# Kernel optimization log

Measured on AMD Instinct MI355X. Metric: run time of the kernel, lower is better.

Reference implementation:

```python
import jax, jax.numpy as jnp
import numpy as np

E, H = 300, 256          # embedding_dim, GRU hidden per direction
D = 2 * H                # BiGRU output / GCN feature dim
V, PAD = 30000, 0
B, T_LEN, C_LEN = 128, 50, 200
N_GCN = 2
OUT = 3


def _gru_dir(x, Wih, Whh, bih, bhh):
    # x: [B,S,E] -> [B,S,H]; torch GRU equations
    h0 = jnp.zeros((x.shape[0], Whh.shape[1]), x.dtype)
    def step(h, xt):
        gi = xt @ Wih.T + bih                 # [B,3H]
        gh = h @ Whh.T + bhh
        ir, iz, inn = jnp.split(gi, 3, axis=-1)
        hr, hz, hn = jnp.split(gh, 3, axis=-1)
        r = jax.nn.sigmoid(ir + hr)
        z = jax.nn.sigmoid(iz + hz)
        n = jnp.tanh(inn + r * hn)
        hnew = (1.0 - z) * n + z * h
        return hnew, hnew
    _, hs = jax.lax.scan(step, h0, jnp.swapaxes(x, 0, 1))
    return jnp.swapaxes(hs, 0, 1)


def _bigru(x, wih, whh, bih, bhh):
    # wih:[2,3H,E] whh:[2,3H,H] bih/bhh:[2,3H]
    f = _gru_dir(x, wih[0], whh[0], bih[0], bhh[0])
    b = _gru_dir(x[:, ::-1], wih[1], whh[1], bih[1], bhh[1])[:, ::-1]
    return jnp.concatenate([f, b], axis=-1)   # [B,S,2H]


def _stance_attn(tgt_emb, clm_emb, gt, gc):
    tgt_ht = _bigru(tgt_emb, *gt)
    clm_ht = _bigru(clm_emb, *gc)
    tgt_last = tgt_ht[:, -1]
    # 'dot' attention: weight[b,c] = claim_ht[b,c] . target_last_ht[b]
    w = jnp.einsum('bcd,bd->bc', clm_ht, tgt_last)
    # NOTE: original `weight.masked_fill(mask==0, -1e9)` result is DISCARDED
    # (non-inplace torch op), so the mask has no effect -> faithfully omitted.
    return tgt_ht, clm_ht, jax.nn.softmax(w, axis=1)


def _gcn(tgt_ht, clm_ht, Ws):
    # StanceGCN: cat nodes, N_GCN layers of dot-correlation attention + residual relu
    node = jnp.concatenate([tgt_ht, clm_ht], axis=1)   # [B,N,D]
    T = tgt_ht.shape[1]
    for i in range(Ws.shape[0]):
        # dot correlation reduces to pairwise inner products (no [B,N,N,D] blowup);
        # `corr_score.masked_fill(adj==0,...)` is also discarded in the source.
        corr = jax.nn.softmax(jnp.einsum('bid,bjd->bij', node, node), axis=2)
        trans = jnp.einsum('bnd,ed->bne', node, Ws[i])  # Linear(bias=False)
        node = jax.nn.relu(node + jnp.einsum('bij,bjd->bid', corr, trans))
    return node[:, :T], node[:, T:]


def setup_inputs() -> dict:
    key = jax.random.key(0)
    ks = iter(jax.random.split(key, 64))
    def norm(shape, s=0.05):
        return (jax.random.normal(next(ks), shape, jnp.float32) * s)
    d = {}
    d['task_id'] = 0
    d['task_target'] = jax.random.randint(next(ks), (B, T_LEN), 0, V)
    d['shared_target'] = jax.random.randint(next(ks), (B, T_LEN), 0, V)
    d['task_claim'] = jax.random.randint(next(ks), (B, C_LEN), 0, V)
    d['shared_claim'] = jax.random.randint(next(ks), (B, C_LEN), 0, V)
    d['task_mask'] = jax.random.randint(next(ks), (B, C_LEN), 0, 2).astype(jnp.int32)
    d['shared_mask'] = jax.random.randint(next(ks), (B, C_LEN), 0, 2).astype(jnp.int32)
    N = T_LEN + C_LEN
    d['task_adj'] = jax.random.randint(next(ks), (B, N, N), 0, 2).astype(jnp.int32)
    d['shared_adj'] = jax.random.randint(next(ks), (B, N, N), 0, 2).astype(jnp.int32)
    d['emb'] = norm((V, E), 0.1).at[PAD].set(0.0)
    for g in ['tgt', 'tgc', 'sgt', 'sgc']:
        d[g + '_wih'] = norm((2, 3 * H, E))
        d[g + '_whh'] = norm((2, 3 * H, H))
        d[g + '_bih'] = norm((2, 3 * H))
        d[g + '_bhh'] = norm((2, 3 * H))
    d['gcn_task_W'] = norm((N_GCN, D, D))
    d['gcn_shared_W'] = norm((N_GCN, D, D))
    d['lin_W'] = norm((OUT, 2 * D))
    d['lin_b'] = norm((OUT,))
    return d


def reference(task_id, task_target, shared_target, task_claim, shared_claim,
              task_mask, shared_mask, task_adj, shared_adj,
              emb,
              tgt_wih, tgt_whh, tgt_bih, tgt_bhh,
              tgc_wih, tgc_whh, tgc_bih, tgc_bhh,
              sgt_wih, sgt_whh, sgt_bih, sgt_bhh,
              sgc_wih, sgc_whh, sgc_bih, sgc_bhh,
              gcn_task_W, gcn_shared_W, lin_W, lin_b):
    # embedding lookups (eval mode: all dropouts are identity)
    tt, tc = emb[task_target], emb[task_claim]
    st, sc = emb[shared_target], emb[shared_claim]
    t_tgt, t_clm, t_w = _stance_attn(tt, tc,
                                     (tgt_wih, tgt_whh, tgt_bih, tgt_bhh),
                                     (tgc_wih, tgc_whh, tgc_bih, tgc_bhh))
    s_tgt, s_clm, s_w = _stance_attn(st, sc,
                                     (sgt_wih, sgt_whh, sgt_bih, sgt_bhh),
                                     (sgc_wih, sgc_whh, sgc_bih, sgc_bhh))
    _, t_clm_rep = _gcn(t_tgt, t_clm, gcn_task_W)
    _, s_clm_rep = _gcn(s_tgt, s_clm, gcn_shared_W)
    # StanceLinear: attention-weighted claim pooling, concat, final linear
    task_rep = jnp.einsum('bc,bcd->bd', t_w, t_clm_rep)
    shared_rep = jnp.einsum('bc,bcd->bd', s_w, s_clm_rep)
    final = jnp.concatenate([task_rep, shared_rep], axis=1)   # [B, 4H+4H]
    return final @ lin_W.T + lin_b                            # [B, 3]
```

## Files before the change

kernel.cpp:

```cpp
#include <hip/hip_runtime.h>
#include <hip/hip_bf16.h>

namespace {

constexpr int B_  = 128;
constexpr int TL  = 50, CL = 200, NNODE = 250;
constexpr int H_  = 256, D_ = 512;
constexpr long NODE_ELE = 128L * 250 * 512;

typedef __attribute__((ext_vector_type(8))) short bf16x8;
typedef __attribute__((ext_vector_type(4))) float f32x4;

__device__ inline float bits2f(unsigned v) { union { unsigned u; float f; } c; c.u = v; return c.f; }
__device__ inline unsigned f2bits(float x) { union { float f; unsigned u; } c; c.f = x; return c.u; }
__device__ inline unsigned short bfbits(float x) {
  __hip_bfloat16 b = __float2bfloat16(x);
  return *(unsigned short*)&b;
}
__device__ inline float bfsel(uint2 v, int r) {
  unsigned w = (r < 2) ? v.x : v.y;
  return bits2f((r & 1) ? (w & 0xFFFF0000u) : (w << 16));
}
__device__ inline float sigf(float x)  { return 1.f / (1.f + __expf(-x)); }
__device__ inline float tanhf_(float x){ return 1.f - 2.f / (__expf(2.f * x) + 1.f); }

struct BGemmArgs {
  const __hip_bfloat16* A; const __hip_bfloat16* B;
  const int* idx; const float* bias; const __hip_bfloat16* Res;
  void* C;
  long aStride, bStride, biasStride, cStride, rStride;
  int M, N, Kreal, lda, ldb, ldc, zShiftA;
};

template<bool GATHER, int OUT>
__global__ __launch_bounds__(256) void bgemm_k(BGemmArgs g) {
  __shared__ __align__(16) __hip_bfloat16 As[128 * 64];
  __shared__ __align__(16) __hip_bfloat16 Bs[128 * 64];
  const int z = blockIdx.z;
  const int m0 = blockIdx.x * 128, n0 = blockIdx.y * 128;
  const int tid = threadIdx.x;
  const int lane = tid & 63, wv = tid >> 6;
  const int wr = wv >> 1, wc = wv & 1;
  const __hip_bfloat16* Ab = GATHER ? g.A : g.A + (long)(z >> g.zShiftA) * g.aStride;
  const __hip_bfloat16* Bb = g.B + (long)z * g.bStride;
  const int sr = tid >> 3, so = tid & 7;
  f32x4 acc[4][4];
  #pragma unroll
  for (int i = 0; i < 4; ++i)
    #pragma unroll
    for (int j = 0; j < 4; ++j) acc[i][j] = (f32x4){0.f, 0.f, 0.f, 0.f};

  const int ktiles = (g.Kreal + 63) >> 6;
  for (int kt = 0; kt < ktiles; ++kt) {
    const int k0 = kt * 64;
    __syncthreads();
    #pragma unroll
    for (int p = 0; p < 4; ++p) {
      int r = p * 32 + sr;
      int row = m0 + r;
      int kg = k0 + so * 8;
      uint4 v = make_uint4(0, 0, 0, 0);
      if (row < g.M && kg + 8 <= g.Kreal) {
        long ao = GATHER ? (long)g.idx[row] * g.lda : (long)row * g.lda;
        v = *(const uint4*)(Ab + ao + kg);
      }
      *(uint4*)((char*)As + ((r * 128 + so * 16) ^ ((r & 7) << 4))) = v;
    }
    #pragma unroll
    for (int p = 0; p < 4; ++p) {
      int r = p * 32 + sr;
      int row = n0 + r;
      int kg = k0 + so * 8;
      uint4 v = make_uint4(0, 0, 0, 0);
      if (row < g.N && kg + 8 <= g.Kreal)
        v = *(const uint4*)(Bb + (long)row * g.ldb + kg);
      *(uint4*)((char*)Bs + ((r * 128 + so * 16) ^ ((r & 7) << 4))) = v;
    }
    __syncthreads();
    #pragma unroll
    for (int ks = 0; ks < 2; ++ks) {
      bf16x8 af[4], bfr[4];
      #pragma unroll
      for (int i = 0; i < 4; ++i) {
        int ra = wr * 64 + i * 16 + (lane & 15);
        af[i] = *(const bf16x8*)((const char*)As +
                 ((ra * 128 + ks * 64 + (lane >> 4) * 16) ^ ((ra & 7) << 4)));
        int rb = wc * 64 + i * 16 + (lane & 15);
        bfr[i] = *(const bf16x8*)((const char*)Bs +
                 ((rb * 128 + ks * 64 + (lane >> 4) * 16) ^ ((rb & 7) << 4)));
      }
      #pragma unroll
      for (int i = 0; i < 4; ++i)
        #pragma unroll
        for (int j = 0; j < 4; ++j)
          acc[i][j] = __builtin_amdgcn_mfma_f32_16x16x32_bf16(af[i], bfr[j], acc[i][j], 0, 0, 0);
    }
  }
  const long cz = (long)z * g.cStride;
  #pragma unroll
  for (int i = 0; i < 4; ++i) {
    int rbase = m0 + wr * 64 + i * 16 + ((lane >> 4) << 2);
    #pragma unroll
    for (int j = 0; j < 4; ++j) {
      int col = n0 + wc * 64 + j * 16 + (lane & 15);
      #pragma unroll
      for (int r = 0; r < 4; ++r) {
        int row = rbase + r;
        float v = acc[i][j][r];
        if (OUT == 0) {
          if (row < g.M && col < g.N)
            ((float*)g.C)[cz + (long)row * g.ldc + col] = v;
        } else if (OUT == 1) {
          if (row < g.M && col < g.N) {
            v += g.bias[(long)z * g.biasStride + col];
            ((__hip_bfloat16*)g.C)[cz + (long)row * g.ldc + col] = __float2bfloat16(v);
          }
        } else if (OUT == 3) {
          if (row < g.M)
            ((__hip_bfloat16*)g.C)[cz + (long)row * g.ldc + col] =
                __float2bfloat16(col < g.N ? v : 0.f);
        } else {
          if (row < g.M && col < g.N) {
            v += __bfloat162float(g.Res[(long)z * g.rStride + (long)row * g.ldc + col]);
            v = fmaxf(v, 0.f);
            ((__hip_bfloat16*)g.C)[cz + (long)row * g.ldc + col] = __float2bfloat16(v);
          }
        }
      }
    }
  }
}

struct PrepArgs {
  const float* whh[4];
  const float* gcnW[2];
  const float* emb;
  const float* wih[4];
  const float* bih[4];
  const float* bhh[4];
  __hip_bfloat16 *whhbf, *gcnWbf, *embbf;
  __hip_bfloat16* wihbf[4];
  float* biasC;
};

constexpr long PR0 = 1572864;
constexpr long PR1 = PR0 + 1048576;
constexpr long PR2 = PR1 + 9120000;
constexpr long PR3 = PR2 + 1867776;
constexpr long PR4 = PR3 + 6144;

__global__ __launch_bounds__(256) void prep_k(PrepArgs a) {
  long i = (long)blockIdx.x * 256 + threadIdx.x;
  if (i >= PR4) return;
  if (i < PR0) {
    int zz = (int)(i / 196608);
    long rem = i - (long)zz * 196608;
    a.whhbf[i] = __float2bfloat16(a.whh[zz >> 1][(long)(zz & 1) * 196608 + rem]);
  } else if (i < PR1) {
    long j = i - PR0;
    a.gcnWbf[j] = __float2bfloat16(a.gcnW[j / 524288][j % 524288]);
  } else if (i < PR2) {
    long j = i - PR1;
    long r = j / 304;
    int c = (int)(j - r * 304);
    a.embbf[j] = __float2bfloat16(c < 300 ? a.emb[r * 300 + c] : 0.f);
  } else if (i < PR3) {
    long j = i - PR2;
    int w = (int)(j / 466944);
    long k = j - (long)w * 466944;
    long r = k / 304;
    int c = (int)(k - r * 304);
    a.wihbf[w][k] = __float2bfloat16(c < 300 ? a.wih[w][r * 300 + c] : 0.f);
  } else {
    long j = i - PR3;
    int w = (int)(j / 1536);
    int k = (int)(j - (long)w * 1536);
    a.biasC[(long)w * 1536 + k] = a.bih[w][k] + ((k % 768) < 512 ? a.bhh[w][k] : 0.f);
  }
}

struct RecArgs {
  const __hip_bfloat16* whhbf;
  const __hip_bfloat16* gi[4];
  const float* bhh[4];
  __hip_bfloat16* nodebf;
};

__global__ __launch_bounds__(512, 2) void gru_rec_k(RecArgs a) {
  __shared__ __align__(16) char hbuf[2][8192];
  const int z = blockIdx.z;
  const int side = z >> 2, sq = (z >> 1) & 1, dir = z & 1;
  const int gidx = side * 2 + sq;
  const int T = sq ? CL : TL;
  const int toff = sq ? TL : 0;
  const __hip_bfloat16* gi = a.gi[gidx] + (long)dir * B_ * T * 768;
  const float* bhh = a.bhh[gidx] + dir * 768;
  const __hip_bfloat16* whh = a.whhbf + (long)z * 768 * 256;
  __hip_bfloat16* nodeb = a.nodebf + (long)side * NODE_ELE;
  const int b0 = blockIdx.x * 16;
  const int tid = threadIdx.x;
  const int lane = tid & 63, wv = tid >> 6;
  const int bcol = lane & 15, g4 = lane >> 4;
  const int u0 = wv * 32 + g4 * 4;
  const int swzh = (bcol & 15) << 4;

  bf16x8 Af[3][2][8];
  #pragma unroll
  for (int g = 0; g < 3; ++g)
    #pragma unroll
    for (int h = 0; h < 2; ++h)
      #pragma unroll
      for (int kt = 0; kt < 8; ++kt) {
        int row = g * 256 + wv * 32 + h * 16 + bcol;
        int col = kt * 32 + g4 * 8;
        Af[g][h][kt] = *(const bf16x8*)(whh + (long)row * 256 + col);
      }
  *(uint4*)&hbuf[0][tid * 16] = make_uint4(0, 0, 0, 0);
  const float4 bn0 = *(const float4*)&bhh[512 + u0];
  const float4 bn1 = *(const float4*)&bhh[512 + u0 + 16];
  __syncthreads();

  const __hip_bfloat16* gip = gi + ((long)(b0 + bcol) * T + (dir ? T - 1 : 0)) * 768 + u0;
  __hip_bfloat16* np = nodeb + ((long)(b0 + bcol) * NNODE + toff + (dir ? T - 1 : 0)) * D_
                       + dir * H_ + u0;
  const long gistep = dir ? -768L : 768L;
  const long nstep  = dir ? -(long)D_ : (long)D_;
  int cur = 0;

  float hreg[2][4];
  #pragma unroll
  for (int h = 0; h < 2; ++h)
    #pragma unroll
    for (int r = 0; r < 4; ++r) hreg[h][r] = 0.f;

  uint2 gv[3][2];
  #pragma unroll
  for (int g = 0; g < 3; ++g)
    #pragma unroll
    for (int h = 0; h < 2; ++h)
      gv[g][h] = *(const uint2*)(gip + g * 256 + h * 16);

  for (int t = 0; t < T; ++t) {
    const char* hib = &hbuf[cur][0];
    f32x4 c[3][2];
    #pragma unroll
    for (int g = 0; g < 3; ++g)
      #pragma unroll
      for (int h = 0; h < 2; ++h) c[g][h] = (f32x4){0.f, 0.f, 0.f, 0.f};
    const int rb = bcol * 512 + g4 * 16;
    #pragma unroll
    for (int kt = 0; kt < 8; ++kt) {
      bf16x8 bh = *(const bf16x8*)(hib + ((rb + kt * 64) ^ swzh));
      #pragma unroll
      for (int g = 0; g < 3; ++g)
        #pragma unroll
        for (int h = 0; h < 2; ++h)
          c[g][h] = __builtin_amdgcn_mfma_f32_16x16x32_bf16(Af[g][h][kt], bh, c[g][h], 0, 0, 0);
    }

    #pragma unroll
    for (int h = 0; h < 2; ++h) {
      float4 bn = h ? bn1 : bn0;
      #pragma unroll
      for (int r = 0; r < 4; ++r) {
        float bnv = (r == 0) ? bn.x : (r == 1) ? bn.y : (r == 2) ? bn.z : bn.w;
        float rr = sigf(bfsel(gv[0][h], r) + c[0][h][r]);
        float zz = sigf(bfsel(gv[1][h], r) + c[1][h][r]);
        float nn = tanhf_(bfsel(gv[2][h], r) + rr * (c[2][h][r] + bnv));
        hreg[h][r] = (1.f - zz) * nn + zz * hreg[h][r];
      }
    }

    {
      const __hip_bfloat16* gn = (t + 1 < T) ? gip + gistep : gip;
      gip = gn;
      #pragma unroll
      for (int g = 0; g < 3; ++g)
        #pragma unroll
        for (int h = 0; h < 2; ++h)
          gv[g][h] = *(const uint2*)(gn + g * 256 + h * 16);
    }

    const int ob0 = bcol * 512 + u0 * 2;
    char* hibn = &hbuf[cur ^ 1][0];
    #pragma unroll
    for (int h = 0; h < 2; ++h) {
      unsigned hb[4];
      #pragma unroll
      for (int r = 0; r < 4; ++r)
        hb[r] = (f2bits(hreg[h][r]) + 0x8000u) & 0xFFFF0000u;
      uint2 hiw;
      hiw.x = (hb[0] >> 16) | hb[1];
      hiw.y = (hb[2] >> 16) | hb[3];
      *(uint2*)(np + h * 16) = hiw;
      *(uint2*)(hibn + ((ob0 + h * 32) ^ swzh)) = hiw;
    }
    np += nstep;
    asm volatile("s_waitcnt lgkmcnt(0)" ::: "memory");
    __builtin_amdgcn_sched_barrier(0);
    __builtin_amdgcn_s_barrier();
    cur ^= 1;
  }
}

__global__ __launch_bounds__(256) void attn_k(const __hip_bfloat16* nodeAll,
                                              float* wT, float* wS) {
  int b = blockIdx.x, side = blockIdx.y;
  const __hip_bfloat16* node = nodeAll + (long)side * NODE_ELE;
  float* w = side ? wS : wT;
  __shared__ float tl[512];
  __shared__ float sc[CL];
  int tid = threadIdx.x;
  {
    const __hip_bfloat16* tr = node + ((long)b * NNODE + (TL - 1)) * D_;
    tl[tid]       = __bfloat162float(tr[tid]);
    tl[tid + 256] = __bfloat162float(tr[tid + 256]);
  }
  __syncthreads();
  int wid = tid >> 6, lane = tid & 63;
  for (int c = wid; c < CL; c += 4) {
    const __hip_bfloat16* row = node + ((long)b * NNODE + TL + c) * D_;
    uint4 v = *(const uint4*)(row + lane * 8);
    const float* tp = &tl[lane * 8];
    float acc = bits2f(v.x << 16)         * tp[0] + bits2f(v.x & 0xFFFF0000u) * tp[1]
              + bits2f(v.y << 16)         * tp[2] + bits2f(v.y & 0xFFFF0000u) * tp[3]
              + bits2f(v.z << 16)         * tp[4] + bits2f(v.z & 0xFFFF0000u) * tp[5]
              + bits2f(v.w << 16)         * tp[6] + bits2f(v.w & 0xFFFF0000u) * tp[7];
    #pragma unroll
    for (int o = 32; o; o >>= 1) acc += __shfl_xor(acc, o, 64);
    if (lane == 0) sc[c] = acc;
  }
  __syncthreads();
  if (wid == 0) {
    float v[4]; float m = -1e30f;
    #pragma unroll
    for (int i = 0; i < 4; ++i) {
      int c = lane + 64 * i;
      v[i] = (c < CL) ? sc[c] : -1e30f;
      m = fmaxf(m, v[i]);
    }
    #pragma unroll
    for (int o = 32; o; o >>= 1) m = fmaxf(m, __shfl_xor(m, o, 64));
    float s = 0.f;
    #pragma unroll
    for (int i = 0; i < 4; ++i) {
      int c = lane + 64 * i;
      v[i] = (c < CL) ? expf(v[i] - m) : 0.f;
      s += v[i];
    }
    #pragma unroll
    for (int o = 32; o; o >>= 1) s += __shfl_xor(s, o, 64);
    float inv = 1.f / s;
    #pragma unroll
    for (int i = 0; i < 4; ++i) {
      int c = lane + 64 * i;
      if (c < CL) w[(long)b * CL + c] = v[i] * inv;
    }
  }
}

__global__ __launch_bounds__(256) void softmaxbf_k(const float* in, __hip_bfloat16* out) {
  int row = blockIdx.x * 4 + (threadIdx.x >> 6);
  int lane = threadIdx.x & 63;
  const float* p = in + (long)row * 256;
  __hip_bfloat16* q = out + (long)row * 256;
  float v[4]; float m = -1e30f;
  #pragma unroll
  for (int i = 0; i < 4; ++i) {
    int c = lane + i * 64;
    v[i] = (c < 250) ? p[c] : -1e30f;
    m = fmaxf(m, v[i]);
  }
  #pragma unroll
  for (int o = 32; o; o >>= 1) m = fmaxf(m, __shfl_xor(m, o, 64));
  float s = 0.f;
  #pragma unroll
  for (int i = 0; i < 4; ++i) {
    int c = lane + i * 64;
    if (c < 250) { v[i] = __expf(v[i] - m); s += v[i]; }
  }
  #pragma unroll
  for (int o = 32; o; o >>= 1) s += __shfl_xor(s, o, 64);
  float inv = 1.f / s;
  #pragma unroll
  for (int i = 0; i < 4; ++i) {
    int c = lane + i * 64;
    q[c] = __float2bfloat16((c < 250) ? v[i] * inv : 0.f);
  }
}

__global__ __launch_bounds__(256) void rep_k(const __hip_bfloat16* nodeAll,
                                             const float* wT, const float* wS,
                                             float* rep) {
  int b = blockIdx.x, side = blockIdx.y;
  const __hip_bfloat16* node = nodeAll + (long)side * NODE_ELE;
  const float* w = side ? wS : wT;
  __shared__ float wl[CL];
  int tid = threadIdx.x;
  if (tid < CL) wl[tid] = w[(long)b * CL + tid];
  __syncthreads();
  #pragma unroll
  for (int h = 0; h < 2; ++h) {
    int d = tid + h * 256;
    float acc = 0.f;
    for (int c = 0; c < CL; ++c)
      acc = fmaf(wl[c], __bfloat162float(node[((long)b * NNODE + TL + c) * D_ + d]), acc);
    rep[((long)side * B_ + b) * D_ + d] = acc;
  }
}

__global__ __launch_bounds__(256) void final_k(const float* rep, const float* linW,
                                               const float* linb, float* out) {
  int b = blockIdx.x, tid = threadIdx.x;
  float a0 = 0.f, a1 = 0.f, a2 = 0.f;
  for (int d = tid; d < 1024; d += 256) {
    float x = rep[(long)(d >> 9) * (B_ * D_) + (long)b * D_ + (d & 511)];
    a0 = fmaf(x, linW[d], a0);
    a1 = fmaf(x, linW[1024 + d], a1);
    a2 = fmaf(x, linW[2048 + d], a2);
  }
  #pragma unroll
  for (int o = 32; o; o >>= 1) {
    a0 += __shfl_xor(a0, o, 64);
    a1 += __shfl_xor(a1, o, 64);
    a2 += __shfl_xor(a2, o, 64);
  }
  __shared__ float red[3][4];
  int wid = tid >> 6, lane = tid & 63;
  if (lane == 0) { red[0][wid] = a0; red[1][wid] = a1; red[2][wid] = a2; }
  __syncthreads();
  if (tid == 0) {
    out[b * 3 + 0] = red[0][0] + red[0][1] + red[0][2] + red[0][3] + linb[0];
    out[b * 3 + 1] = red[1][0] + red[1][1] + red[1][2] + red[1][3] + linb[1];
    out[b * 3 + 2] = red[2][0] + red[2][1] + red[2][2] + red[2][3] + linb[2];
  }
}

__global__ void diag_k(float* out, int n, float v) {
  int i = blockIdx.x * blockDim.x + threadIdx.x;
  if (i < n) out[i] = v;
}

}

extern "C" void kernel_launch(void* const* d_in, const int* in_sizes, int n_in,
                              void* d_out, int out_size, void* d_ws, size_t ws_size,
                              hipStream_t stream) {
  const int* task_target   = (const int*)d_in[1];
  const int* shared_target = (const int*)d_in[2];
  const int* task_claim    = (const int*)d_in[3];
  const int* shared_claim  = (const int*)d_in[4];
  const float* emb      = (const float*)d_in[9];
  const float* tgt_wih  = (const float*)d_in[10];
  const float* tgt_whh  = (const float*)d_in[11];
  const float* tgt_bih  = (const float*)d_in[12];
  const float* tgt_bhh  = (const float*)d_in[13];
  const float* tgc_wih  = (const float*)d_in[14];
  const float* tgc_whh  = (const float*)d_in[15];
  const float* tgc_bih  = (const float*)d_in[16];
  const float* tgc_bhh  = (const float*)d_in[17];
  const float* sgt_wih  = (const float*)d_in[18];
  const float* sgt_whh  = (const float*)d_in[19];
  const float* sgt_bih  = (const float*)d_in[20];
  const float* sgt_bhh  = (const float*)d_in[21];
  const float* sgc_wih  = (const float*)d_in[22];
  const float* sgc_whh  = (const float*)d_in[23];
  const float* sgc_bih  = (const float*)d_in[24];
  const float* sgc_bhh  = (const float*)d_in[25];
  const float* gcnW_task   = (const float*)d_in[26];
  const float* gcnW_shared = (const float*)d_in[27];
  const float* linW = (const float*)d_in[28];
  const float* linb = (const float*)d_in[29];
  float* out = (float*)d_out;

  const size_t SZ_WHH   = 3145728;
  const size_t SZ_GCNW  = 2097152;
  const size_t SZ_BIASC = 24576;
  const size_t SZ_ARENA = 196608000;
  const size_t SZ_NODE  = 65536000;
  const size_t SZ_W     = 102400;
  const size_t SZ_REP   = 524288;
  const size_t NEED = SZ_WHH + SZ_GCNW + SZ_BIASC + SZ_ARENA + SZ_NODE
                      + 2 * SZ_W + SZ_REP + 4096;

  if (ws_size < NEED) {
    diag_k<<<(out_size + 255) / 256, 256, 0, stream>>>(out, out_size,
                                                       (float)(ws_size >> 20));
    return;
  }

  char* p = (char*)d_ws;
  auto alloc = [&](size_t bytes) { char* r = p; p += (bytes + 255) & ~(size_t)255; return r; };
  __hip_bfloat16* whhbf  = (__hip_bfloat16*)alloc(SZ_WHH);
  __hip_bfloat16* gcnWbf = (__hip_bfloat16*)alloc(SZ_GCNW);
  float* biasC = (float*)alloc(SZ_BIASC);
  char* arena  = alloc(SZ_ARENA);
  char* nodeC  = alloc(SZ_NODE);
  float* wT    = (float*)alloc(SZ_W);
  float* wS    = (float*)alloc(SZ_W);
  float* rep   = (float*)alloc(SZ_REP);
  __hip_bfloat16* nodebf = (__hip_bfloat16*)nodeC;

  __hip_bfloat16* gi_tt = (__hip_bfloat16*)(arena);
  __hip_bfloat16* gi_tc = (__hip_bfloat16*)(arena + 19660800);
  __hip_bfloat16* gi_st = (__hip_bfloat16*)(arena + 98304000);
  __hip_bfloat16* gi_sc = (__hip_bfloat16*)(arena + 117964800);
  __hip_bfloat16* embbf = (__hip_bfloat16*)(nodeC);
  __hip_bfloat16* wihbf[4] = {
    (__hip_bfloat16*)(nodeC + 18240000),
    (__hip_bfloat16*)(nodeC + 19173888),
    (__hip_bfloat16*)(nodeC + 20107776),
    (__hip_bfloat16*)(nodeC + 21041664)};
  __hip_bfloat16* tmpbf  = (__hip_bfloat16*)(arena);
  __hip_bfloat16* corrbf = (__hip_bfloat16*)(arena + 65536000);
  float*          corrF  = (float*)(arena + 98304000);
  __hip_bfloat16* transT = (__hip_bfloat16*)(arena + 98304000);

  {
    PrepArgs pa;
    pa.whh[0] = tgt_whh; pa.whh[1] = tgc_whh; pa.whh[2] = sgt_whh; pa.whh[3] = sgc_whh;
    pa.gcnW[0] = gcnW_task; pa.gcnW[1] = gcnW_shared;
    pa.emb = emb;
    pa.wih[0] = tgt_wih; pa.wih[1] = tgc_wih; pa.wih[2] = sgt_wih; pa.wih[3] = sgc_wih;
    pa.bih[0] = tgt_bih; pa.bih[1] = tgc_bih; pa.bih[2] = sgt_bih; pa.bih[3] = sgc_bih;
    pa.bhh[0] = tgt_bhh; pa.bhh[1] = tgc_bhh; pa.bhh[2] = sgt_bhh; pa.bhh[3] = sgc_bhh;
    pa.whhbf = whhbf; pa.gcnWbf = gcnWbf; pa.embbf = embbf;
    pa.wihbf[0] = wihbf[0]; pa.wihbf[1] = wihbf[1];
    pa.wihbf[2] = wihbf[2]; pa.wihbf[3] = wihbf[3];
    pa.biasC = biasC;
    prep_k<<<(int)((PR4 + 255) / 256), 256, 0, stream>>>(pa);
  }

  auto proj = [&](const int* idx, __hip_bfloat16* wih, const float* bias,
                  __hip_bfloat16* gi, int Mrows, int gx) {
    BGemmArgs ga{};
    ga.A = embbf; ga.idx = idx; ga.B = wih; ga.bias = bias; ga.C = gi;
    ga.aStride = 0; ga.bStride = 768L * 304; ga.biasStride = 768;
    ga.cStride = (long)Mrows * 768; ga.zShiftA = 0;
    ga.M = Mrows; ga.N = 768; ga.Kreal = 304; ga.lda = 304; ga.ldb = 304; ga.ldc = 768;
    bgemm_k<true, 1><<<dim3(gx, 6, 2), 256, 0, stream>>>(ga);
  };
  proj(task_target,   wihbf[0], biasC,        gi_tt, 6400, 50);
  proj(task_claim,    wihbf[1], biasC + 1536, gi_tc, 25600, 200);
  proj(shared_target, wihbf[2], biasC + 3072, gi_st, 6400, 50);
  proj(shared_claim,  wihbf[3], biasC + 4608, gi_sc, 25600, 200);

  RecArgs ra;
  ra.whhbf = whhbf;
  ra.gi[0] = gi_tt; ra.gi[1] = gi_tc; ra.gi[2] = gi_st; ra.gi[3] = gi_sc;
  ra.bhh[0] = tgt_bhh; ra.bhh[1] = tgc_bhh; ra.bhh[2] = sgt_bhh; ra.bhh[3] = sgc_bhh;
  ra.nodebf = nodebf;
  gru_rec_k<<<dim3(8, 1, 8), 512, 0, stream>>>(ra);

  attn_k<<<dim3(128, 2), 256, 0, stream>>>(nodebf, wT, wS);

  for (int layer = 0; layer < 2; ++layer) {
    const __hip_bfloat16* inbf = layer ? tmpbf : nodebf;
    BGemmArgs ca{};
    ca.A = inbf; ca.B = inbf; ca.C = corrF;
    ca.aStride = 128000; ca.bStride = 128000; ca.cStride = 64000; ca.zShiftA = 0;
    ca.M = 250; ca.N = 250; ca.Kreal = 512; ca.lda = 512; ca.ldb = 512; ca.ldc = 256;
    bgemm_k<false, 0><<<dim3(2, 2, 256), 256, 0, stream>>>(ca);
    softmaxbf_k<<<16000, 256, 0, stream>>>(corrF, corrbf);
    BGemmArgs ta{};
    ta.A = gcnWbf + (long)layer * 262144; ta.B = inbf; ta.C = transT;
    ta.aStride = 524288; ta.bStride = 128000; ta.cStride = 131072; ta.zShiftA = 7;
    ta.M = 512; ta.N = 250; ta.Kreal = 512; ta.lda = 512; ta.ldb = 512; ta.ldc = 256;
    bgemm_k<false, 3><<<dim3(4, 2, 256), 256, 0, stream>>>(ta);
    BGemmArgs aa{};
    aa.A = corrbf; aa.B = transT; aa.Res = inbf;
    aa.C = layer ? (void*)nodebf : (void*)tmpbf;
    aa.aStride = 64000; aa.bStride = 131072; aa.cStride = 128000;
    aa.rStride = 128000; aa.zShiftA = 0;
    aa.M = 250; aa.N = 512; aa.Kreal = 256; aa.lda = 256; aa.ldb = 256; aa.ldc = 512;
    bgemm_k<false, 5><<<dim3(2, 4, 256), 256, 0, stream>>>(aa);
  }

  rep_k<<<dim3(128, 2), 256, 0, stream>>>(nodebf, wT, wS, rep);
  final_k<<<dim3(128), 256, 0, stream>>>(rep, linW, linb, out);
}
```

Before: 1.660 ms.

## Double-buffer bgemm with direct global-to-LDS loads and pad K to 320

The bf16 GEMM now uses two LDS buffers filled by global_load_lds, which writes global data straight into shared memory. The next K tile is prefetched while MFMAs run on the current one, and the per-tile pre-sync and register staging are removed. The embedding and input-weight padding grows from 304 to 320 columns so K divides evenly by 64, which allows dropping the bounds checks. The cost is more padded compute and memory. Row bounds checks are also removed, so any other caller whose M or N is not a multiple of 128 could read out of bounds.

```diff
diff --git a/kernel.cpp b/kernel.cpp
--- a/kernel.cpp
+++ b/kernel.cpp
@@ -34,8 +34,8 @@
 
 template<bool GATHER, int OUT>
 __global__ __launch_bounds__(256) void bgemm_k(BGemmArgs g) {
-  __shared__ __align__(16) __hip_bfloat16 As[128 * 64];
-  __shared__ __align__(16) __hip_bfloat16 Bs[128 * 64];
+  __shared__ __align__(16) char As[2][16384];
+  __shared__ __align__(16) char Bs[2][16384];
   const int z = blockIdx.z;
   const int m0 = blockIdx.x * 128, n0 = blockIdx.y * 128;
   const int tid = threadIdx.x;
@@ -43,51 +43,63 @@
   const int wr = wv >> 1, wc = wv & 1;
   const __hip_bfloat16* Ab = GATHER ? g.A : g.A + (long)(z >> g.zShiftA) * g.aStride;
   const __hip_bfloat16* Bb = g.B + (long)z * g.bStride;
-  const int sr = tid >> 3, so = tid & 7;
+
+  long asrc[4], bsrc[4];
+  int ldso[4];
+  #pragma unroll
+  for (int c2 = 0; c2 < 4; ++c2) {
+    int o = c2 * 256 + tid;
+    int row = o >> 3, ko = o & 7;
+    int colel = 8 * (ko ^ (row & 7));
+    long arow = GATHER ? (long)g.idx[m0 + row] * g.lda : (long)(m0 + row) * g.lda;
+    asrc[c2] = arow + colel;
+    bsrc[c2] = (long)(n0 + row) * g.ldb + colel;
+    ldso[c2] = o * 16;
+  }
+
   f32x4 acc[4][4];
   #pragma unroll
   for (int i = 0; i < 4; ++i)
     #pragma unroll
     for (int j = 0; j < 4; ++j) acc[i][j] = (f32x4){0.f, 0.f, 0.f, 0.f};
 
-  const int ktiles = (g.Kreal + 63) >> 6;
-  for (int kt = 0; kt < ktiles; ++kt) {
-    const int k0 = kt * 64;
-    __syncthreads();
-    #pragma unroll
-    for (int p = 0; p < 4; ++p) {
-      int r = p * 32 + sr;
-      int row = m0 + r;
-      int kg = k0 + so * 8;
-      uint4 v = make_uint4(0, 0, 0, 0);
-      if (row < g.M && kg + 8 <= g.Kreal) {
-        long ao = GATHER ? (long)g.idx[row] * g.lda : (long)row * g.lda;
-        v = *(const uint4*)(Ab + ao + kg);
+  const int KT = g.Kreal >> 6;
+  #pragma unroll
+  for (int c2 = 0; c2 < 4; ++c2) {
+    __builtin_amdgcn_global_load_lds(
+        (const __attribute__((address_space(1))) unsigned*)(Ab + asrc[c2]),
+        (__attribute__((address_space(3))) unsigned*)(&As[0][0] + ldso[c2]), 16, 0, 0);
+    __builtin_amdgcn_global_load_lds(
+        (const __attribute__((address_space(1))) unsigned*)(Bb + bsrc[c2]),
+        (__attribute__((address_space(3))) unsigned*)(&Bs[0][0] + ldso[c2]), 16, 0, 0);
+  }
+  __syncthreads();
+
+  int buf = 0;
+  for (int kt = 0; kt < KT; ++kt) {
+    if (kt + 1 < KT) {
+      long ko = (long)(kt + 1) * 64;
+      #pragma unroll
+      for (int c2 = 0; c2 < 4; ++c2) {
+        __builtin_amdgcn_global_load_lds(
+            (const __attribute__((address_space(1))) unsigned*)(Ab + asrc[c2] + ko),
+            (__attribute__((address_space(3))) unsigned*)(&As[buf ^ 1][0] + ldso[c2]), 16, 0, 0);
+        __builtin_amdgcn_global_load_lds(
+            (const __attribute__((address_space(1))) unsigned*)(Bb + bsrc[c2] + ko),
+            (__attribute__((address_space(3))) unsigned*)(&Bs[buf ^ 1][0] + ldso[c2]), 16, 0, 0);
       }
-      *(uint4*)((char*)As + ((r * 128 + so * 16) ^ ((r & 7) << 4))) = v;
-    }
-    #pragma unroll
-    for (int p = 0; p < 4; ++p) {
-      int r = p * 32 + sr;
-      int row = n0 + r;
-      int kg = k0 + so * 8;
-      uint4 v = make_uint4(0, 0, 0, 0);
-      if (row < g.N && kg + 8 <= g.Kreal)
-        v = *(const uint4*)(Bb + (long)row * g.ldb + kg);
-      *(uint4*)((char*)Bs + ((r * 128 + so * 16) ^ ((r & 7) << 4))) = v;
-    }
-    __syncthreads();
+    }
+    const char* ab = &As[buf][0];
+    const char* bb = &Bs[buf][0];
     #pragma unroll
     for (int ks = 0; ks < 2; ++ks) {
       bf16x8 af[4], bfr[4];
       #pragma unroll
       for (int i = 0; i < 4; ++i) {
         int ra = wr * 64 + i * 16 + (lane & 15);
-        af[i] = *(const bf16x8*)((const char*)As +
-                 ((ra * 128 + ks * 64 + (lane >> 4) * 16) ^ ((ra & 7) << 4)));
+        af[i] = *(const bf16x8*)(ab + ((ra * 128 + ks * 64 + (lane >> 4) * 16) ^ ((ra & 7) << 4)));
         int rb = wc * 64 + i * 16 + (lane & 15);
-        bfr[i] = *(const bf16x8*)((const char*)Bs +
-                 ((rb * 128 + ks * 64 + (lane >> 4) * 16) ^ ((rb & 7) << 4)));
+        bfr[i] = *(const bf16x8*)(bb + ((rb * 128 + ks * 64 + (lane >> 4) * 16) ^ ((rb & 7) << 4)));
       }
       #pragma unroll
       for (int i = 0; i < 4; ++i)
@@ -95,7 +107,10 @@
         for (int j = 0; j < 4; ++j)
           acc[i][j] = __builtin_amdgcn_mfma_f32_16x16x32_bf16(af[i], bfr[j], acc[i][j], 0, 0, 0);
     }
-  }
+    __syncthreads();
+    buf ^= 1;
+  }
+
   const long cz = (long)z * g.cStride;
   #pragma unroll
   for (int i = 0; i < 4; ++i) {
@@ -145,8 +160,8 @@
 
 constexpr long PR0 = 1572864;
 constexpr long PR1 = PR0 + 1048576;
-constexpr long PR2 = PR1 + 9120000;
-constexpr long PR3 = PR2 + 1867776;
+constexpr long PR2 = PR1 + 9600000;
+constexpr long PR3 = PR2 + 1966080;
 constexpr long PR4 = PR3 + 6144;
 
 __global__ __launch_bounds__(256) void prep_k(PrepArgs a) {
@@ -161,15 +176,15 @@
     a.gcnWbf[j] = __float2bfloat16(a.gcnW[j / 524288][j % 524288]);
   } else if (i < PR2) {
     long j = i - PR1;
-    long r = j / 304;
-    int c = (int)(j - r * 304);
+    long r = j / 320;
+    int c = (int)(j - r * 320);
     a.embbf[j] = __float2bfloat16(c < 300 ? a.emb[r * 300 + c] : 0.f);
   } else if (i < PR3) {
     long j = i - PR2;
-    int w = (int)(j / 466944);
-    long k = j - (long)w * 466944;
-    long r = k / 304;
-    int c = (int)(k - r * 304);
+    int w = (int)(j / 491520);
+    long k = j - (long)w * 491520;
+    long r = k / 320;
+    int c = (int)(k - r * 320);
     a.wihbf[w][k] = __float2bfloat16(c < 300 ? a.wih[w][r * 300 + c] : 0.f);
   } else {
     long j = i - PR3;
@@ -507,10 +522,10 @@
   __hip_bfloat16* gi_sc = (__hip_bfloat16*)(arena + 117964800);
   __hip_bfloat16* embbf = (__hip_bfloat16*)(nodeC);
   __hip_bfloat16* wihbf[4] = {
-    (__hip_bfloat16*)(nodeC + 18240000),
-    (__hip_bfloat16*)(nodeC + 19173888),
-    (__hip_bfloat16*)(nodeC + 20107776),
-    (__hip_bfloat16*)(nodeC + 21041664)};
+    (__hip_bfloat16*)(nodeC + 19200000),
+    (__hip_bfloat16*)(nodeC + 20183040),
+    (__hip_bfloat16*)(nodeC + 21166080),
+    (__hip_bfloat16*)(nodeC + 22149120)};
   __hip_bfloat16* tmpbf  = (__hip_bfloat16*)(arena);
   __hip_bfloat16* corrbf = (__hip_bfloat16*)(arena + 65536000);
   float*          corrF  = (float*)(arena + 98304000);
@@ -535,9 +550,9 @@
                   __hip_bfloat16* gi, int Mrows, int gx) {
     BGemmArgs ga{};
     ga.A = embbf; ga.idx = idx; ga.B = wih; ga.bias = bias; ga.C = gi;
-    ga.aStride = 0; ga.bStride = 768L * 304; ga.biasStride = 768;
+    ga.aStride = 0; ga.bStride = 768L * 320; ga.biasStride = 768;
     ga.cStride = (long)Mrows * 768; ga.zShiftA = 0;
-    ga.M = Mrows; ga.N = 768; ga.Kreal = 304; ga.lda = 304; ga.ldb = 304; ga.ldc = 768;
+    ga.M = Mrows; ga.N = 768; ga.Kreal = 320; ga.lda = 320; ga.ldb = 320; ga.ldc = 768;
     bgemm_k<true, 1><<<dim3(gx, 6, 2), 256, 0, stream>>>(ga);
   };
   proj(task_target,   wihbf[0], biasC,        gi_tt, 6400, 50);
```

After: 1.527 ms. 1.09x faster.
